# Performance work log

Measured on AMD Instinct MI355X. Metric: run time of the kernel, lower is better.

## Reference

```python
import jax, jax.numpy as jnp
import numpy as np

N_RAYS = 8192
N_SAMPLES = 128
HIDDEN = 128
SH_DIM = 16
RAY_EXT_FACTOR = 10.0


def rsh_cart_3(d):
    # Real spherical harmonics up to degree 3, Cartesian form (16 coeffs).
    x, y, z = d[..., 0], d[..., 1], d[..., 2]
    x2, y2, z2 = x * x, y * y, z * z
    xy, yz, xz = x * y, y * z, x * z
    return jnp.stack([
        0.282094791773878 * jnp.ones_like(x),
        -0.48860251190292 * y,
        0.48860251190292 * z,
        -0.48860251190292 * x,
        1.0925484305920792 * xy,
        -1.0925484305920792 * yz,
        0.94617469575756 * z2 - 0.31539156525252,
        -1.0925484305920792 * xz,
        0.5462742152960396 * (x2 - y2),
        0.5900435899266435 * y * (-3.0 * x2 + y2),
        2.8906114426405538 * xy * z,
        0.4570457994644658 * y * (1.0 - 5.0 * z2),
        0.3731763325901154 * z * (5.0 * z2 - 3.0),
        0.4570457994644658 * x * (1.0 - 5.0 * z2),
        1.445305721320277 * z * (x2 - y2),
        0.5900435899266435 * x * (-x2 + 3.0 * y2),
    ], axis=-1)


def setup_inputs() -> dict:
    key = jax.random.key(0)
    ks = jax.random.split(key, 11)
    o = jax.random.normal(ks[0], (N_RAYS, 3), dtype=jnp.float32)
    origins = 2.5 * o / jnp.linalg.norm(o, axis=-1, keepdims=True)
    # aim roughly at the unit AABB so most rays are active
    dirs = -origins + 0.2 * jax.random.normal(ks[1], (N_RAYS, 3), dtype=jnp.float32)
    u = jax.random.uniform(ks[2], (N_RAYS, N_SAMPLES), dtype=jnp.float32)
    s1 = 1.0 / np.sqrt(3.0)
    s2 = 1.0 / np.sqrt(HIDDEN)
    s3 = 1.0 / np.sqrt(HIDDEN + SH_DIM)
    return {
        'origins': origins,
        'dirs': dirs,
        'u': u,
        'W1': s1 * jax.random.normal(ks[3], (3, HIDDEN), dtype=jnp.float32),
        'b1': jnp.zeros((HIDDEN,), jnp.float32),
        'W2': s2 * jax.random.normal(ks[4], (HIDDEN, HIDDEN), dtype=jnp.float32),
        'b2': jnp.zeros((HIDDEN,), jnp.float32),
        'Wd': s2 * jax.random.normal(ks[5], (HIDDEN, 1), dtype=jnp.float32),
        'bd': jnp.zeros((1,), jnp.float32),
        'Wc': s3 * jax.random.normal(ks[6], (HIDDEN + SH_DIM, 3), dtype=jnp.float32),
        'bc': jnp.zeros((3,), jnp.float32),
    }


def reference(origins, dirs, u, W1, b1, W2, b2, Wd, bd, Wc, bc):
    B, T = u.shape
    # ---- AABB ([-1,1]^3) slab intersection -> tnear/tfar, active mask ----
    inv_d = 1.0 / dirs
    t1 = (-1.0 - origins) * inv_d
    t2 = (1.0 - origins) * inv_d
    tnear = jnp.maximum(jnp.max(jnp.minimum(t1, t2), axis=-1), 0.0)  # (B,)
    tfar = jnp.min(jnp.maximum(t1, t2), axis=-1)                      # (B,)
    active = tfar > tnear                                             # (B,)
    tfar_c = jnp.maximum(tfar, tnear + 1e-3)
    # ---- stratified ray step sampling ----
    frac = (jnp.arange(T, dtype=u.dtype) + u) / T                     # (B,T)
    ts = tnear[:, None] + (tfar_c - tnear)[:, None] * frac            # (B,T)
    xyz = origins[:, None, :] + dirs[:, None, :] * ts[..., None]      # (B,T,3)
    # aabb is [-1,1]^3 so ndc == xyz; spatial filter = bounds test
    xyz_ndc = xyz
    mask = jnp.all(jnp.abs(xyz_ndc) <= 1.0, axis=-1) & active[:, None]  # (B,T)
    dnorm = jnp.linalg.norm(dirs, axis=-1)                            # (B,)
    ynm = rsh_cart_3(dirs / dnorm[:, None])                           # (B,16)
    # ---- radiance field MLP over all sample points ----
    x = xyz_ndc.reshape(B * T, 3)
    h = jax.nn.relu(x @ W1 + b1)
    h = jax.nn.relu(h @ W2 + b2)
    sigma = jax.nn.softplus(h @ Wd + bd).reshape(B, T)
    cond = jnp.broadcast_to(ynm[:, None, :], (B, T, SH_DIM)).reshape(B * T, SH_DIM)
    color = jax.nn.sigmoid(jnp.concatenate([h, cond], axis=-1) @ Wc + bc).reshape(B, T, 3)
    # zero out points rejected by the spatial filter (torch writes only masked)
    sigma = sigma * mask
    color = color * mask[..., None]
    # ---- transmittance integration (integrate_timesteps) ----
    tfinal = tfar_c * RAY_EXT_FACTOR
    deltas = jnp.diff(ts, axis=-1, append=tfinal[:, None])            # (B,T)
    sd = sigma * deltas * dnorm[:, None]
    csum = jnp.cumsum(sd, axis=-1)
    # weights_i = T_i * alpha_i = exp(-csum_{i-1}) - exp(-csum_i)
    weights = jnp.exp(sd - csum) - jnp.exp(-csum)                     # (B,T)
    color_out = jnp.einsum('bt,btc->bc', weights, color)              # (B,3)
    alpha_out = jnp.sum(weights, axis=-1, keepdims=True)              # (B,1)
    rgba = jnp.concatenate([color_out, alpha_out], axis=-1)           # (B,4)
    return jnp.where(active[:, None], rgba, 0.0)
```

## Files before the change

### kernel.cpp

```cpp
#include <hip/hip_runtime.h>
#include <math.h>

#define NRAYS 8192
#define T 128
#define H 128
#define SHD 16

using short8 = __attribute__((ext_vector_type(8))) short;
using f32x4  = __attribute__((ext_vector_type(4))) float;
using f32x2  = __attribute__((ext_vector_type(2))) float;
using u32x2  = __attribute__((ext_vector_type(2))) unsigned;

__device__ __forceinline__ float fexp(float x) {
  return exp2f(x * 1.44269504088896341f);
}
__device__ __forceinline__ float softplus_f(float x) {
  return fmaxf(x, 0.f) + 0.693147180559945309f * log2f(1.f + fexp(-fabsf(x)));
}
__device__ __forceinline__ float sigmoid_f(float x) {
  return __builtin_amdgcn_rcpf(1.f + fexp(-x));
}

__device__ __forceinline__ unsigned f2bf(float f) {
  unsigned u = __float_as_uint(f);
  return (u + 0x7fffu + ((u >> 16) & 1u)) >> 16;
}

__device__ __forceinline__ unsigned pk2(f32x2 h) {
  unsigned r;
  asm("v_cvt_pk_bf16_f32 %0, %1, %2" : "=v"(r) : "v"(h[0]), "v"(h[1]));
  return r;
}

__global__ void preprocess(const float* __restrict__ W2, const float* __restrict__ Wd,
                           const float* __restrict__ Wc, const float* __restrict__ bc,
                           const float* __restrict__ origins, const float* __restrict__ dirs,
                           unsigned short* __restrict__ w2t,
                           unsigned short* __restrict__ woutf,
                           float* __restrict__ rayp_all) {
  const int t = blockIdx.x * 256 + threadIdx.x;
  if (t < 16384) {
    const int n = t >> 7, p = t & 127;
    const int o = (p >> 3) ^ (n & 7);
    const int k = o * 8 + (p & 7);
    w2t[t] = (unsigned short)f2bf(W2[k * 128 + n]);
  }
  if (t < 2048) {
    const int kk = t >> 9, L = (t >> 3) & 63, j = t & 7;
    const int c = L & 15, g = L >> 4;
    const int k = kk * 32 + g * 8 + j;
    float v = 0.f;
    if (c == 0) v = Wd[k];
    else if (c < 4) v = Wc[k * 3 + (c - 1)];
    woutf[t] = (unsigned short)f2bf(v);
  }
  if (t < NRAYS) {
    const float ox = origins[t*3+0], oy = origins[t*3+1], oz = origins[t*3+2];
    const float dx = dirs[t*3+0],  dy = dirs[t*3+1],  dz = dirs[t*3+2];
    const float ix = 1.f/dx, iy = 1.f/dy, iz = 1.f/dz;
    const float t1x = (-1.f-ox)*ix, t2x = (1.f-ox)*ix;
    const float t1y = (-1.f-oy)*iy, t2y = (1.f-oy)*iy;
    const float t1z = (-1.f-oz)*iz, t2z = (1.f-oz)*iz;
    float tnear = fmaxf(fmaxf(fminf(t1x,t2x), fminf(t1y,t2y)), fminf(t1z,t2z));
    tnear = fmaxf(tnear, 0.f);
    const float tfar = fminf(fminf(fmaxf(t1x,t2x), fmaxf(t1y,t2y)), fmaxf(t1z,t2z));
    const bool  active = tfar > tnear;
    const float tfar_c = fmaxf(tfar, tnear + 1e-3f);
    const float dnorm = sqrtf(dx*dx + dy*dy + dz*dz);
    const float nx = dx/dnorm, ny = dy/dnorm, nz = dz/dnorm;
    const float x2 = nx*nx, y2 = ny*ny, z2 = nz*nz;
    const float xy = nx*ny, yz = ny*nz, xz = nx*nz;
    float ynm[16];
    ynm[0]  = 0.282094791773878f;
    ynm[1]  = -0.48860251190292f*ny;
    ynm[2]  = 0.48860251190292f*nz;
    ynm[3]  = -0.48860251190292f*nx;
    ynm[4]  = 1.0925484305920792f*xy;
    ynm[5]  = -1.0925484305920792f*yz;
    ynm[6]  = 0.94617469575756f*z2 - 0.31539156525252f;
    ynm[7]  = -1.0925484305920792f*xz;
    ynm[8]  = 0.5462742152960396f*(x2-y2);
    ynm[9]  = 0.5900435899266435f*ny*(-3.f*x2+y2);
    ynm[10] = 2.8906114426405538f*xy*nz;
    ynm[11] = 0.4570457994644658f*ny*(1.f-5.f*z2);
    ynm[12] = 0.3731763325901154f*nz*(5.f*z2-3.f);
    ynm[13] = 0.4570457994644658f*nx*(1.f-5.f*z2);
    ynm[14] = 1.445305721320277f*nz*(x2-y2);
    ynm[15] = 0.5900435899266435f*nx*(-x2+3.f*y2);
    float cp0 = bc[0], cp1 = bc[1], cp2 = bc[2];
    #pragma unroll
    for (int s = 0; s < SHD; ++s) {
      cp0 = fmaf(ynm[s], Wc[(H+s)*3+0], cp0);
      cp1 = fmaf(ynm[s], Wc[(H+s)*3+1], cp1);
      cp2 = fmaf(ynm[s], Wc[(H+s)*3+2], cp2);
    }
    rayp_all[t*8+0] = tfar_c;
    rayp_all[t*8+1] = dnorm;
    rayp_all[t*8+2] = active ? 1.f : 0.f;
    rayp_all[t*8+3] = cp0;
    rayp_all[t*8+4] = cp1;
    rayp_all[t*8+5] = cp2;
    rayp_all[t*8+6] = tnear;
    rayp_all[t*8+7] = 0.f;
  }
}

__global__ __launch_bounds__(256, 4) void nerf_render(
    const float* __restrict__ origins, const float* __restrict__ dirs,
    const float* __restrict__ u, const float* __restrict__ W1,
    const float* __restrict__ b1, const float* __restrict__ b2,
    const float* __restrict__ bd, const unsigned short* __restrict__ w2t,
    const unsigned short* __restrict__ woutf, const float* __restrict__ rayp_all,
    float* __restrict__ out)
{
  const int ray = blockIdx.x;
  const int tid = threadIdx.x;
  const int L = tid & 63;
  const int w = tid >> 6;
  const int g = L >> 4;
  const int c = L & 15;

  __shared__ __align__(16) short Bs[16384];
  __shared__ __align__(16) float baseA[H];
  __shared__ __align__(16) float slopeA[H];
  __shared__ float ts_s[T];
  __shared__ float mask_s[T];
  __shared__ float wred[2][4];
  __shared__ float wtot[2];

  const float tfar_c = rayp_all[ray*8+0];
  const float dnorm  = rayp_all[ray*8+1];
  const float actf   = rayp_all[ray*8+2];
  const float cpo0   = rayp_all[ray*8+3];
  const float cpo1   = rayp_all[ray*8+4];
  const float cpo2   = rayp_all[ray*8+5];
  const float tnear  = rayp_all[ray*8+6];

  {
    const float4* src = (const float4*)w2t;
    float4* dst = (float4*)Bs;
    #pragma unroll
    for (int i = 0; i < 8; ++i) dst[tid + i * 256] = src[tid + i * 256];
  }

  if (tid < T) {
    const int tl = tid;
    const float ox = origins[ray*3+0], oy = origins[ray*3+1], oz = origins[ray*3+2];
    const float dx = dirs[ray*3+0],  dy = dirs[ray*3+1],  dz = dirs[ray*3+2];
    const bool active = actf != 0.f;
    const float ut = u[ray*T + tl];
    const float frac = ((float)tl + ut) * (1.f/(float)T);
    const float tt = tnear + (tfar_c - tnear) * frac;
    const float px = fmaf(dx, tt, ox);
    const float py = fmaf(dy, tt, oy);
    const float pz = fmaf(dz, tt, oz);
    ts_s[tl] = tt;
    const bool m = (fabsf(px) <= 1.f) && (fabsf(py) <= 1.f) && (fabsf(pz) <= 1.f) && active;
    mask_s[tl] = m ? 1.f : 0.f;
    const float w0 = W1[tl], w1v = W1[H + tl], w2v = W1[2*H + tl];
    baseA[tl]  = fmaf(ox, w0, fmaf(oy, w1v, fmaf(oz, w2v, b1[tl])));
    slopeA[tl] = fmaf(dx, w0, fmaf(dy, w1v, dz * w2v));
  }

  f32x4 acc[2][8];
  #pragma unroll
  for (int mt = 0; mt < 8; ++mt) {
    const float4 bv = *(const float4*)&b2[mt*16 + g*4];
    #pragma unroll
    for (int tm = 0; tm < 2; ++tm) {
      acc[tm][mt][0] = bv.x; acc[tm][mt][1] = bv.y;
      acc[tm][mt][2] = bv.z; acc[tm][mt][3] = bv.w;
    }
  }
  __syncthreads();

  const float t0 = ts_s[32*w + c];
  const float t1 = ts_s[32*w + 16 + c];
  const f32x2 tz0 = {t0, t0}, tz1 = {t1, t1};
  const f32x2 zero2 = {0.f, 0.f};

  #pragma unroll
  for (int ks = 0; ks < 4; ++ks) {
    const int kb = ks*32 + g*8;
    const f32x4 bq0 = *(const f32x4*)&baseA[kb];
    const f32x4 bq1 = *(const f32x4*)&baseA[kb+4];
    const f32x4 sq0 = *(const f32x4*)&slopeA[kb];
    const f32x4 sq1 = *(const f32x4*)&slopeA[kb+4];
    const f32x2 b01 = {bq0[0], bq0[1]}, b23 = {bq0[2], bq0[3]};
    const f32x2 b45 = {bq1[0], bq1[1]}, b67 = {bq1[2], bq1[3]};
    const f32x2 s01 = {sq0[0], sq0[1]}, s23 = {sq0[2], sq0[3]};
    const f32x2 s45 = {sq1[0], sq1[1]}, s67 = {sq1[2], sq1[3]};
    const f32x2 a01 = __builtin_elementwise_max(__builtin_elementwise_fma(tz0, s01, b01), zero2);
    const f32x2 a23 = __builtin_elementwise_max(__builtin_elementwise_fma(tz0, s23, b23), zero2);
    const f32x2 a45 = __builtin_elementwise_max(__builtin_elementwise_fma(tz0, s45, b45), zero2);
    const f32x2 a67 = __builtin_elementwise_max(__builtin_elementwise_fma(tz0, s67, b67), zero2);
    const f32x2 e01 = __builtin_elementwise_max(__builtin_elementwise_fma(tz1, s01, b01), zero2);
    const f32x2 e23 = __builtin_elementwise_max(__builtin_elementwise_fma(tz1, s23, b23), zero2);
    const f32x2 e45 = __builtin_elementwise_max(__builtin_elementwise_fma(tz1, s45, b45), zero2);
    const f32x2 e67 = __builtin_elementwise_max(__builtin_elementwise_fma(tz1, s67, b67), zero2);
    union U { uint4 u; short8 s; } A0, A1;
    A0.u = make_uint4(pk2(a01), pk2(a23), pk2(a45), pk2(a67));
    A1.u = make_uint4(pk2(e01), pk2(e23), pk2(e45), pk2(e67));
    const int swb = ((ks*4 + g) ^ (c & 7)) * 8;
    #pragma unroll
    for (int mt = 0; mt < 8; ++mt) {
      const short8 wf = *(const short8*)&Bs[(mt*16 + c)*128 + swb];
      acc[0][mt] = __builtin_amdgcn_mfma_f32_16x16x32_bf16(wf, A0.s, acc[0][mt], 0, 0, 0);
      acc[1][mt] = __builtin_amdgcn_mfma_f32_16x16x32_bf16(wf, A1.s, acc[1][mt], 0, 0, 0);
    }
  }
  __syncthreads();
  float4* SredP = (float4*)Bs;
  short*  As2   = Bs + 2048;

  short* As2w = As2 + w * 640;
  short8 wa[4];
  #pragma unroll
  for (int kk = 0; kk < 4; ++kk)
    wa[kk] = *(const short8*)&woutf[(kk*64 + L)*8];

  #pragma unroll
  for (int tm = 0; tm < 2; ++tm) {
    f32x4 oacc;
    oacc[0] = 0.f; oacc[1] = 0.f; oacc[2] = 0.f; oacc[3] = 0.f;
    #pragma unroll
    for (int kk = 0; kk < 4; ++kk) {
      #pragma unroll
      for (int i = 0; i < 2; ++i) {
        const f32x4 a = acc[tm][kk*2 + i];
        const f32x2 h01 = __builtin_elementwise_max((f32x2){a[0], a[1]}, zero2);
        const f32x2 h23 = __builtin_elementwise_max((f32x2){a[2], a[3]}, zero2);
        *(uint2*)&As2w[c*40 + i*16 + g*4] = make_uint2(pk2(h01), pk2(h23));
      }
      const short8 hbf = *(const short8*)&As2w[c*40 + g*8];
      oacc = __builtin_amdgcn_mfma_f32_16x16x32_bf16(wa[kk], hbf, oacc, 0, 0, 0);
    }
    if (g == 0)
      SredP[32*w + 16*tm + c] = make_float4(oacc[0], oacc[1], oacc[2], oacc[3]);
  }
  __syncthreads();

  float sd = 0.f, cc0 = 0.f, cc1 = 0.f, cc2 = 0.f;
  if (tid < T) {
    const float4 sv = SredP[tid];
    const float mk = mask_s[tid];
    const float sigma = softplus_f(sv.x + bd[0]) * mk;
    cc0 = mk * sigmoid_f(sv.y + cpo0);
    cc1 = mk * sigmoid_f(sv.z + cpo1);
    cc2 = mk * sigmoid_f(sv.w + cpo2);
    const float tt = ts_s[tid];
    const float tnext = (tid < T-1) ? ts_s[tid + 1] : tfar_c * 10.f;
    sd = sigma * (tnext - tt) * dnorm;
  }

  float val = sd;
  #pragma unroll
  for (int off = 1; off < 64; off <<= 1) {
    const float tmp = __shfl_up(val, off);
    if (L >= off) val += tmp;
  }
  if (tid < T && L == 63) wtot[w] = val;
  __syncthreads();
  const float csum = val + ((w == 1) ? wtot[0] : 0.f);

  float wgt = 0.f, wcx = 0.f, wcy = 0.f, wcz = 0.f;
  if (tid < T) {
    wgt = fexp(sd - csum) - fexp(-csum);
    wcx = wgt * cc0; wcy = wgt * cc1; wcz = wgt * cc2;
  }
  #pragma unroll
  for (int mm = 32; mm >= 1; mm >>= 1) {
    wgt += __shfl_xor(wgt, mm);
    wcx += __shfl_xor(wcx, mm);
    wcy += __shfl_xor(wcy, mm);
    wcz += __shfl_xor(wcz, mm);
  }
  if (tid < T && L == 0) {
    wred[w][0] = wgt; wred[w][1] = wcx; wred[w][2] = wcy; wred[w][3] = wcz;
  }
  __syncthreads();
  if (tid == 0) {
    const float aw = wred[0][0] + wred[1][0];
    const float o0 = wred[0][1] + wred[1][1];
    const float o1 = wred[0][2] + wred[1][2];
    const float o2 = wred[0][3] + wred[1][3];
    const bool act = actf != 0.f;
    out[ray*4+0] = act ? o0 : 0.f;
    out[ray*4+1] = act ? o1 : 0.f;
    out[ray*4+2] = act ? o2 : 0.f;
    out[ray*4+3] = act ? aw : 0.f;
  }
}

extern "C" void kernel_launch(void* const* d_in, const int* in_sizes, int n_in,
                              void* d_out, int out_size, void* d_ws, size_t ws_size,
                              hipStream_t stream) {
  const float* origins = (const float*)d_in[0];
  const float* dirs    = (const float*)d_in[1];
  const float* u       = (const float*)d_in[2];
  const float* W1      = (const float*)d_in[3];
  const float* b1      = (const float*)d_in[4];
  const float* W2      = (const float*)d_in[5];
  const float* b2      = (const float*)d_in[6];
  const float* Wd      = (const float*)d_in[7];
  const float* bd      = (const float*)d_in[8];
  const float* Wc      = (const float*)d_in[9];
  const float* bc      = (const float*)d_in[10];

  unsigned short* w2t      = (unsigned short*)d_ws;
  unsigned short* woutf    = (unsigned short*)((char*)d_ws + 32768);
  float*          rayp_all = (float*)((char*)d_ws + 36864);

  preprocess<<<64, 256, 0, stream>>>(W2, Wd, Wc, bc, origins, dirs,
                                     w2t, woutf, rayp_all);
  nerf_render<<<NRAYS, 256, 0, stream>>>(origins, dirs, u, W1, b1, b2, bd,
                                         w2t, woutf, rayp_all, (float*)d_out);
}
```

Before: 133.2 us.

## Map one ray per wavefront and amortize W2 LDS staging across four rays

Each block now handles four rays, one per wavefront, instead of one ray per block. This spreads the 32KB W2 copy into shared memory over four rays, and the per-ray setup, scan and reduction now run inside one wavefront with shuffles and ds_bpermute, so most block-level barriers are gone. Each wave walks its 128 samples in four chunks of 32 and carries a running cumulative sum through a per-chunk prefix scan. The cost is more serial work per wave, more bpermute traffic to rebuild layer-1 activations, and a grid four times smaller.

```diff
diff --git a/kernel.cpp b/kernel.cpp
--- a/kernel.cpp
+++ b/kernel.cpp
@@ -9,7 +9,6 @@
 using short8 = __attribute__((ext_vector_type(8))) short;
 using f32x4  = __attribute__((ext_vector_type(4))) float;
 using f32x2  = __attribute__((ext_vector_type(2))) float;
-using u32x2  = __attribute__((ext_vector_type(2))) unsigned;
 
 __device__ __forceinline__ float fexp(float x) {
   return exp2f(x * 1.44269504088896341f);
@@ -30,6 +29,14 @@
   unsigned r;
   asm("v_cvt_pk_bf16_f32 %0, %1, %2" : "=v"(r) : "v"(h[0]), "v"(h[1]));
   return r;
+}
+
+__device__ __forceinline__ float rflf(float v) {
+  return __builtin_bit_cast(float, __builtin_amdgcn_readfirstlane(__builtin_bit_cast(int, v)));
+}
+
+__device__ __forceinline__ float bpermf(int byteaddr, float v) {
+  return __builtin_bit_cast(float, __builtin_amdgcn_ds_bpermute(byteaddr, __builtin_bit_cast(int, v)));
 }
 
 __global__ void preprocess(const float* __restrict__ W2, const float* __restrict__ Wd,
@@ -113,28 +120,16 @@
     const unsigned short* __restrict__ woutf, const float* __restrict__ rayp_all,
     float* __restrict__ out)
 {
-  const int ray = blockIdx.x;
   const int tid = threadIdx.x;
   const int L = tid & 63;
   const int w = tid >> 6;
   const int g = L >> 4;
   const int c = L & 15;
+  const int ray = blockIdx.x * 4 + w;
 
   __shared__ __align__(16) short Bs[16384];
-  __shared__ __align__(16) float baseA[H];
-  __shared__ __align__(16) float slopeA[H];
-  __shared__ float ts_s[T];
-  __shared__ float mask_s[T];
-  __shared__ float wred[2][4];
-  __shared__ float wtot[2];
-
-  const float tfar_c = rayp_all[ray*8+0];
-  const float dnorm  = rayp_all[ray*8+1];
-  const float actf   = rayp_all[ray*8+2];
-  const float cpo0   = rayp_all[ray*8+3];
-  const float cpo1   = rayp_all[ray*8+4];
-  const float cpo2   = rayp_all[ray*8+5];
-  const float tnear  = rayp_all[ray*8+6];
+  __shared__ __align__(16) float b2s[128];
+  __shared__ __align__(16) short As2[4 * 640];
 
   {
     const float4* src = (const float4*)w2t;
@@ -142,153 +137,181 @@
     #pragma unroll
     for (int i = 0; i < 8; ++i) dst[tid + i * 256] = src[tid + i * 256];
   }
-
-  if (tid < T) {
-    const int tl = tid;
-    const float ox = origins[ray*3+0], oy = origins[ray*3+1], oz = origins[ray*3+2];
-    const float dx = dirs[ray*3+0],  dy = dirs[ray*3+1],  dz = dirs[ray*3+2];
-    const bool active = actf != 0.f;
-    const float ut = u[ray*T + tl];
-    const float frac = ((float)tl + ut) * (1.f/(float)T);
-    const float tt = tnear + (tfar_c - tnear) * frac;
+  if (tid < 128) b2s[tid] = b2[tid];
+
+  const float tfar_c = rflf(rayp_all[ray*8+0]);
+  const float dnorm  = rflf(rayp_all[ray*8+1]);
+  const float actf   = rflf(rayp_all[ray*8+2]);
+  const float cp0    = rflf(rayp_all[ray*8+3]);
+  const float cp1    = rflf(rayp_all[ray*8+4]);
+  const float cp2    = rflf(rayp_all[ray*8+5]);
+  const float tnear  = rflf(rayp_all[ray*8+6]);
+  const float bd0    = rflf(bd[0]);
+  const float ox = rflf(origins[ray*3+0]);
+  const float oy = rflf(origins[ray*3+1]);
+  const float oz = rflf(origins[ray*3+2]);
+  const float dx = rflf(dirs[ray*3+0]);
+  const float dy = rflf(dirs[ray*3+1]);
+  const float dz = rflf(dirs[ray*3+2]);
+  const bool active = actf != 0.f;
+
+  float ts_q[2], dmn_q[2], mk_q[2];
+  #pragma unroll
+  for (int q = 0; q < 2; ++q) {
+    const int s = q*64 + L;
+    const float uv = u[ray*T + s];
+    const float frac = ((float)s + uv) * (1.f/(float)T);
+    const float tt = fmaf(tfar_c - tnear, frac, tnear);
+    ts_q[q] = tt;
     const float px = fmaf(dx, tt, ox);
     const float py = fmaf(dy, tt, oy);
     const float pz = fmaf(dz, tt, oz);
-    ts_s[tl] = tt;
-    const bool m = (fabsf(px) <= 1.f) && (fabsf(py) <= 1.f) && (fabsf(pz) <= 1.f) && active;
-    mask_s[tl] = m ? 1.f : 0.f;
-    const float w0 = W1[tl], w1v = W1[H + tl], w2v = W1[2*H + tl];
-    baseA[tl]  = fmaf(ox, w0, fmaf(oy, w1v, fmaf(oz, w2v, b1[tl])));
-    slopeA[tl] = fmaf(dx, w0, fmaf(dy, w1v, dz * w2v));
-  }
-
-  f32x4 acc[2][8];
-  #pragma unroll
-  for (int mt = 0; mt < 8; ++mt) {
-    const float4 bv = *(const float4*)&b2[mt*16 + g*4];
-    #pragma unroll
-    for (int tm = 0; tm < 2; ++tm) {
-      acc[tm][mt][0] = bv.x; acc[tm][mt][1] = bv.y;
-      acc[tm][mt][2] = bv.z; acc[tm][mt][3] = bv.w;
-    }
-  }
-  __syncthreads();
-
-  const float t0 = ts_s[32*w + c];
-  const float t1 = ts_s[32*w + 16 + c];
-  const f32x2 tz0 = {t0, t0}, tz1 = {t1, t1};
-  const f32x2 zero2 = {0.f, 0.f};
-
-  #pragma unroll
-  for (int ks = 0; ks < 4; ++ks) {
-    const int kb = ks*32 + g*8;
-    const f32x4 bq0 = *(const f32x4*)&baseA[kb];
-    const f32x4 bq1 = *(const f32x4*)&baseA[kb+4];
-    const f32x4 sq0 = *(const f32x4*)&slopeA[kb];
-    const f32x4 sq1 = *(const f32x4*)&slopeA[kb+4];
-    const f32x2 b01 = {bq0[0], bq0[1]}, b23 = {bq0[2], bq0[3]};
-    const f32x2 b45 = {bq1[0], bq1[1]}, b67 = {bq1[2], bq1[3]};
-    const f32x2 s01 = {sq0[0], sq0[1]}, s23 = {sq0[2], sq0[3]};
-    const f32x2 s45 = {sq1[0], sq1[1]}, s67 = {sq1[2], sq1[3]};
-    const f32x2 a01 = __builtin_elementwise_max(__builtin_elementwise_fma(tz0, s01, b01), zero2);
-    const f32x2 a23 = __builtin_elementwise_max(__builtin_elementwise_fma(tz0, s23, b23), zero2);
-    const f32x2 a45 = __builtin_elementwise_max(__builtin_elementwise_fma(tz0, s45, b45), zero2);
-    const f32x2 a67 = __builtin_elementwise_max(__builtin_elementwise_fma(tz0, s67, b67), zero2);
-    const f32x2 e01 = __builtin_elementwise_max(__builtin_elementwise_fma(tz1, s01, b01), zero2);
-    const f32x2 e23 = __builtin_elementwise_max(__builtin_elementwise_fma(tz1, s23, b23), zero2);
-    const f32x2 e45 = __builtin_elementwise_max(__builtin_elementwise_fma(tz1, s45, b45), zero2);
-    const f32x2 e67 = __builtin_elementwise_max(__builtin_elementwise_fma(tz1, s67, b67), zero2);
-    union U { uint4 u; short8 s; } A0, A1;
-    A0.u = make_uint4(pk2(a01), pk2(a23), pk2(a45), pk2(a67));
-    A1.u = make_uint4(pk2(e01), pk2(e23), pk2(e45), pk2(e67));
-    const int swb = ((ks*4 + g) ^ (c & 7)) * 8;
-    #pragma unroll
-    for (int mt = 0; mt < 8; ++mt) {
-      const short8 wf = *(const short8*)&Bs[(mt*16 + c)*128 + swb];
-      acc[0][mt] = __builtin_amdgcn_mfma_f32_16x16x32_bf16(wf, A0.s, acc[0][mt], 0, 0, 0);
-      acc[1][mt] = __builtin_amdgcn_mfma_f32_16x16x32_bf16(wf, A1.s, acc[1][mt], 0, 0, 0);
-    }
-  }
-  __syncthreads();
-  float4* SredP = (float4*)Bs;
-  short*  As2   = Bs + 2048;
-
-  short* As2w = As2 + w * 640;
+    mk_q[q] = ((fabsf(px) <= 1.f) && (fabsf(py) <= 1.f) && (fabsf(pz) <= 1.f) && active)
+                ? 1.f : 0.f;
+  }
+  {
+    const float t64 = __shfl(ts_q[1], 0);
+    float tn0 = __shfl(ts_q[0], (L+1) & 63);
+    float tn1 = __shfl(ts_q[1], (L+1) & 63);
+    tn0 = (L == 63) ? t64 : tn0;
+    tn1 = (L == 63) ? tfar_c * 10.f : tn1;
+    dmn_q[0] = mk_q[0] * (tn0 - ts_q[0]) * dnorm;
+    dmn_q[1] = mk_q[1] * (tn1 - ts_q[1]) * dnorm;
+  }
+  float base_q[2], slope_q[2];
+  #pragma unroll
+  for (int q = 0; q < 2; ++q) {
+    const int hh = q*64 + L;
+    const float w0v = W1[hh], w1v = W1[H + hh], w2v = W1[2*H + hh];
+    base_q[q]  = fmaf(ox, w0v, fmaf(oy, w1v, fmaf(oz, w2v, b1[hh])));
+    slope_q[q] = fmaf(dx, w0v, fmaf(dy, w1v, dz * w2v));
+  }
+
   short8 wa[4];
   #pragma unroll
   for (int kk = 0; kk < 4; ++kk)
     wa[kk] = *(const short8*)&woutf[(kk*64 + L)*8];
 
-  #pragma unroll
-  for (int tm = 0; tm < 2; ++tm) {
-    f32x4 oacc;
-    oacc[0] = 0.f; oacc[1] = 0.f; oacc[2] = 0.f; oacc[3] = 0.f;
-    #pragma unroll
-    for (int kk = 0; kk < 4; ++kk) {
+  __syncthreads();
+
+  short* As2w = As2 + w * 640;
+  const int permbase = g * 32;
+  const f32x2 zero2 = {0.f, 0.f};
+  f32x4 acc[2][8];
+  float csum = 0.f, pw = 0.f, pxc = 0.f, pyc = 0.f, pzc = 0.f;
+
+  #pragma unroll
+  for (int stp = 0; stp < 4; ++stp) {
+    const int q = stp >> 1;
+    const int i0 = ((stp*32 + c) & 63) * 4;
+    const int i1 = ((stp*32 + 16 + c) & 63) * 4;
+    const float t0 = bpermf(i0, ts_q[q]);
+    const float t1 = bpermf(i1, ts_q[q]);
+    const float d0 = bpermf(i0, dmn_q[q]);
+    const float d1 = bpermf(i1, dmn_q[q]);
+    const f32x2 tz0 = {t0, t0}, tz1 = {t1, t1};
+
+    #pragma unroll
+    for (int mt = 0; mt < 8; ++mt) {
+      const f32x4 bv = *(const f32x4*)&b2s[mt*16 + g*4];
+      acc[0][mt] = bv; acc[1][mt] = bv;
+    }
+
+    #pragma unroll
+    for (int ks = 0; ks < 4; ++ks) {
+      const int kq = ks >> 1;
+      const int pb = permbase + ((ks & 1) << 7);
+      float bj[8], sj[8];
       #pragma unroll
-      for (int i = 0; i < 2; ++i) {
-        const f32x4 a = acc[tm][kk*2 + i];
-        const f32x2 h01 = __builtin_elementwise_max((f32x2){a[0], a[1]}, zero2);
-        const f32x2 h23 = __builtin_elementwise_max((f32x2){a[2], a[3]}, zero2);
-        *(uint2*)&As2w[c*40 + i*16 + g*4] = make_uint2(pk2(h01), pk2(h23));
+      for (int j = 0; j < 8; ++j) {
+        bj[j] = bpermf(pb + j*4, base_q[kq]);
+        sj[j] = bpermf(pb + j*4, slope_q[kq]);
       }
-      const short8 hbf = *(const short8*)&As2w[c*40 + g*8];
-      oacc = __builtin_amdgcn_mfma_f32_16x16x32_bf16(wa[kk], hbf, oacc, 0, 0, 0);
-    }
-    if (g == 0)
-      SredP[32*w + 16*tm + c] = make_float4(oacc[0], oacc[1], oacc[2], oacc[3]);
-  }
-  __syncthreads();
-
-  float sd = 0.f, cc0 = 0.f, cc1 = 0.f, cc2 = 0.f;
-  if (tid < T) {
-    const float4 sv = SredP[tid];
-    const float mk = mask_s[tid];
-    const float sigma = softplus_f(sv.x + bd[0]) * mk;
-    cc0 = mk * sigmoid_f(sv.y + cpo0);
-    cc1 = mk * sigmoid_f(sv.z + cpo1);
-    cc2 = mk * sigmoid_f(sv.w + cpo2);
-    const float tt = ts_s[tid];
-    const float tnext = (tid < T-1) ? ts_s[tid + 1] : tfar_c * 10.f;
-    sd = sigma * (tnext - tt) * dnorm;
-  }
-
-  float val = sd;
-  #pragma unroll
-  for (int off = 1; off < 64; off <<= 1) {
-    const float tmp = __shfl_up(val, off);
-    if (L >= off) val += tmp;
-  }
-  if (tid < T && L == 63) wtot[w] = val;
-  __syncthreads();
-  const float csum = val + ((w == 1) ? wtot[0] : 0.f);
-
-  float wgt = 0.f, wcx = 0.f, wcy = 0.f, wcz = 0.f;
-  if (tid < T) {
-    wgt = fexp(sd - csum) - fexp(-csum);
-    wcx = wgt * cc0; wcy = wgt * cc1; wcz = wgt * cc2;
-  }
-  #pragma unroll
-  for (int mm = 32; mm >= 1; mm >>= 1) {
-    wgt += __shfl_xor(wgt, mm);
-    wcx += __shfl_xor(wcx, mm);
-    wcy += __shfl_xor(wcy, mm);
-    wcz += __shfl_xor(wcz, mm);
-  }
-  if (tid < T && L == 0) {
-    wred[w][0] = wgt; wred[w][1] = wcx; wred[w][2] = wcy; wred[w][3] = wcz;
-  }
-  __syncthreads();
-  if (tid == 0) {
-    const float aw = wred[0][0] + wred[1][0];
-    const float o0 = wred[0][1] + wred[1][1];
-    const float o1 = wred[0][2] + wred[1][2];
-    const float o2 = wred[0][3] + wred[1][3];
-    const bool act = actf != 0.f;
-    out[ray*4+0] = act ? o0 : 0.f;
-    out[ray*4+1] = act ? o1 : 0.f;
-    out[ray*4+2] = act ? o2 : 0.f;
-    out[ray*4+3] = act ? aw : 0.f;
+      const f32x2 b01 = {bj[0], bj[1]}, b23 = {bj[2], bj[3]};
+      const f32x2 b45 = {bj[4], bj[5]}, b67 = {bj[6], bj[7]};
+      const f32x2 s01 = {sj[0], sj[1]}, s23 = {sj[2], sj[3]};
+      const f32x2 s45 = {sj[4], sj[5]}, s67 = {sj[6], sj[7]};
+      const f32x2 a01 = __builtin_elementwise_max(__builtin_elementwise_fma(tz0, s01, b01), zero2);
+      const f32x2 a23 = __builtin_elementwise_max(__builtin_elementwise_fma(tz0, s23, b23), zero2);
+      const f32x2 a45 = __builtin_elementwise_max(__builtin_elementwise_fma(tz0, s45, b45), zero2);
+      const f32x2 a67 = __builtin_elementwise_max(__builtin_elementwise_fma(tz0, s67, b67), zero2);
+      const f32x2 e01 = __builtin_elementwise_max(__builtin_elementwise_fma(tz1, s01, b01), zero2);
+      const f32x2 e23 = __builtin_elementwise_max(__builtin_elementwise_fma(tz1, s23, b23), zero2);
+      const f32x2 e45 = __builtin_elementwise_max(__builtin_elementwise_fma(tz1, s45, b45), zero2);
+      const f32x2 e67 = __builtin_elementwise_max(__builtin_elementwise_fma(tz1, s67, b67), zero2);
+      union U { uint4 u; short8 s; } A0, A1;
+      A0.u = make_uint4(pk2(a01), pk2(a23), pk2(a45), pk2(a67));
+      A1.u = make_uint4(pk2(e01), pk2(e23), pk2(e45), pk2(e67));
+      const int swb = ((ks*4 + g) ^ (c & 7)) * 8;
+      #pragma unroll
+      for (int mt = 0; mt < 8; ++mt) {
+        const short8 wf = *(const short8*)&Bs[(mt*16 + c)*128 + swb];
+        acc[0][mt] = __builtin_amdgcn_mfma_f32_16x16x32_bf16(wf, A0.s, acc[0][mt], 0, 0, 0);
+        acc[1][mt] = __builtin_amdgcn_mfma_f32_16x16x32_bf16(wf, A1.s, acc[1][mt], 0, 0, 0);
+      }
+    }
+
+    f32x4 osig[2];
+    #pragma unroll
+    for (int tm = 0; tm < 2; ++tm) {
+      f32x4 oacc;
+      oacc[0] = 0.f; oacc[1] = 0.f; oacc[2] = 0.f; oacc[3] = 0.f;
+      #pragma unroll
+      for (int kk = 0; kk < 4; ++kk) {
+        #pragma unroll
+        for (int i = 0; i < 2; ++i) {
+          const f32x4 a = acc[tm][kk*2 + i];
+          const f32x2 h01 = __builtin_elementwise_max((f32x2){a[0], a[1]}, zero2);
+          const f32x2 h23 = __builtin_elementwise_max((f32x2){a[2], a[3]}, zero2);
+          *(uint2*)&As2w[c*40 + i*16 + g*4] = make_uint2(pk2(h01), pk2(h23));
+        }
+        const short8 hbf = *(const short8*)&As2w[c*40 + g*8];
+        oacc = __builtin_amdgcn_mfma_f32_16x16x32_bf16(wa[kk], hbf, oacc, 0, 0, 0);
+      }
+      osig[tm] = oacc;
+    }
+
+    const float sd0 = softplus_f(osig[0][0] + bd0) * d0;
+    const float sd1 = softplus_f(osig[1][0] + bd0) * d1;
+    float p0 = sd0;
+    #pragma unroll
+    for (int off = 1; off < 16; off <<= 1) {
+      const float tpp = __shfl_up(p0, off, 16);
+      p0 += ((L & 15) >= off) ? tpp : 0.f;
+    }
+    const float tot0 = __shfl(p0, 15);
+    float p1 = sd1;
+    #pragma unroll
+    for (int off = 1; off < 16; off <<= 1) {
+      const float tpp = __shfl_up(p1, off, 16);
+      p1 += ((L & 15) >= off) ? tpp : 0.f;
+    }
+    const float tot1 = __shfl(p1, 15);
+    const float cs0 = csum + p0;
+    const float cs1 = csum + tot0 + p1;
+    csum += tot0 + tot1;
+    const float w0 = fexp(sd0 - cs0) - fexp(-cs0);
+    const float w1 = fexp(sd1 - cs1) - fexp(-cs1);
+    pw  += w0 + w1;
+    pxc += w0 * sigmoid_f(osig[0][1] + cp0) + w1 * sigmoid_f(osig[1][1] + cp0);
+    pyc += w0 * sigmoid_f(osig[0][2] + cp1) + w1 * sigmoid_f(osig[1][2] + cp1);
+    pzc += w0 * sigmoid_f(osig[0][3] + cp2) + w1 * sigmoid_f(osig[1][3] + cp2);
+  }
+
+  #pragma unroll
+  for (int off = 1; off < 16; off <<= 1) {
+    pw  += __shfl_xor(pw, off);
+    pxc += __shfl_xor(pxc, off);
+    pyc += __shfl_xor(pyc, off);
+    pzc += __shfl_xor(pzc, off);
+  }
+  if (L == 0) {
+    float4 o;
+    o.x = active ? pxc : 0.f;
+    o.y = active ? pyc : 0.f;
+    o.z = active ? pzc : 0.f;
+    o.w = active ? pw  : 0.f;
+    *(float4*)&out[ray*4] = o;
   }
 }
 
@@ -313,6 +336,6 @@
 
   preprocess<<<64, 256, 0, stream>>>(W2, Wd, Wc, bc, origins, dirs,
                                      w2t, woutf, rayp_all);
-  nerf_render<<<NRAYS, 256, 0, stream>>>(origins, dirs, u, W1, b1, b2, bd,
-                                         w2t, woutf, rayp_all, (float*)d_out);
-}
+  nerf_render<<<NRAYS/4, 256, 0, stream>>>(origins, dirs, u, W1, b1, b2, bd,
+                                           w2t, woutf, rayp_all, (float*)d_out);
+}
```

New measurement: 214.8 us. 1.61x slower.

## Process two rays per 512-thread block and double-buffer output-layer staging

Applied to the files above, without the earlier changes.

Each block now handles two rays with 512 threads, so the 32KB bf16 W2 tile loaded into shared memory is shared by both rays and the per-ray global-to-LDS copy cost is halved. The output-layer staging alternates between two LDS slabs so the next slab can be written while the previous one is consumed by the MFMA. Shared memory per block grows and launch bounds change to 512x2, which may affect occupancy. The final output is written as a single float4.

```diff
diff --git a/kernel.cpp b/kernel.cpp
--- a/kernel.cpp
+++ b/kernel.cpp
@@ -9,7 +9,6 @@
 using short8 = __attribute__((ext_vector_type(8))) short;
 using f32x4  = __attribute__((ext_vector_type(4))) float;
 using f32x2  = __attribute__((ext_vector_type(2))) float;
-using u32x2  = __attribute__((ext_vector_type(2))) unsigned;
 
 __device__ __forceinline__ float fexp(float x) {
   return exp2f(x * 1.44269504088896341f);
@@ -105,7 +104,17 @@
   }
 }
 
-__global__ __launch_bounds__(256, 4) void nerf_render(
+#define SLAB_W(kk, sb) { \
+  { const f32x4 a = acc[tm][(kk)*2+0]; \
+    const f32x2 h01 = __builtin_elementwise_max((f32x2){a[0],a[1]}, zero2); \
+    const f32x2 h23 = __builtin_elementwise_max((f32x2){a[2],a[3]}, zero2); \
+    *(uint2*)&(sb)[c*40 + g*4] = make_uint2(pk2(h01), pk2(h23)); } \
+  { const f32x4 a = acc[tm][(kk)*2+1]; \
+    const f32x2 h01 = __builtin_elementwise_max((f32x2){a[0],a[1]}, zero2); \
+    const f32x2 h23 = __builtin_elementwise_max((f32x2){a[2],a[3]}, zero2); \
+    *(uint2*)&(sb)[c*40 + 16 + g*4] = make_uint2(pk2(h01), pk2(h23)); } }
+
+__global__ __launch_bounds__(512, 2) void nerf_render(
     const float* __restrict__ origins, const float* __restrict__ dirs,
     const float* __restrict__ u, const float* __restrict__ W1,
     const float* __restrict__ b1, const float* __restrict__ b2,
@@ -113,53 +122,50 @@
     const unsigned short* __restrict__ woutf, const float* __restrict__ rayp_all,
     float* __restrict__ out)
 {
-  const int ray = blockIdx.x;
   const int tid = threadIdx.x;
   const int L = tid & 63;
   const int w = tid >> 6;
+  const int wr = w & 3;
+  const int r  = w >> 2;
   const int g = L >> 4;
   const int c = L & 15;
 
   __shared__ __align__(16) short Bs[16384];
-  __shared__ __align__(16) float baseA[H];
-  __shared__ __align__(16) float slopeA[H];
-  __shared__ float ts_s[T];
-  __shared__ float mask_s[T];
-  __shared__ float wred[2][4];
-  __shared__ float wtot[2];
-
-  const float tfar_c = rayp_all[ray*8+0];
-  const float dnorm  = rayp_all[ray*8+1];
-  const float actf   = rayp_all[ray*8+2];
-  const float cpo0   = rayp_all[ray*8+3];
-  const float cpo1   = rayp_all[ray*8+4];
-  const float cpo2   = rayp_all[ray*8+5];
-  const float tnear  = rayp_all[ray*8+6];
+  __shared__ __align__(16) float baseA[2][H];
+  __shared__ __align__(16) float slopeA[2][H];
+  __shared__ __align__(16) float ts_s[2][T];
+  __shared__ __align__(16) float mask_s[2][T];
+  __shared__ float wred[2][2][4];
+  __shared__ float wtot[2][2];
 
   {
     const float4* src = (const float4*)w2t;
     float4* dst = (float4*)Bs;
     #pragma unroll
-    for (int i = 0; i < 8; ++i) dst[tid + i * 256] = src[tid + i * 256];
-  }
-
-  if (tid < T) {
-    const int tl = tid;
-    const float ox = origins[ray*3+0], oy = origins[ray*3+1], oz = origins[ray*3+2];
-    const float dx = dirs[ray*3+0],  dy = dirs[ray*3+1],  dz = dirs[ray*3+2];
+    for (int i = 0; i < 4; ++i) dst[tid + i * 512] = src[tid + i * 512];
+  }
+
+  if (tid < 256) {
+    const int r2 = tid >> 7, tl = tid & 127;
+    const int ray2 = blockIdx.x * 2 + r2;
+    const float tfar_c = rayp_all[ray2*8+0];
+    const float actf   = rayp_all[ray2*8+2];
+    const float tnear  = rayp_all[ray2*8+6];
+    const float ox = origins[ray2*3+0], oy = origins[ray2*3+1], oz = origins[ray2*3+2];
+    const float dx = dirs[ray2*3+0],  dy = dirs[ray2*3+1],  dz = dirs[ray2*3+2];
     const bool active = actf != 0.f;
-    const float ut = u[ray*T + tl];
+    const float ut = u[ray2*T + tl];
     const float frac = ((float)tl + ut) * (1.f/(float)T);
     const float tt = tnear + (tfar_c - tnear) * frac;
     const float px = fmaf(dx, tt, ox);
     const float py = fmaf(dy, tt, oy);
     const float pz = fmaf(dz, tt, oz);
-    ts_s[tl] = tt;
+    ts_s[r2][tl] = tt;
     const bool m = (fabsf(px) <= 1.f) && (fabsf(py) <= 1.f) && (fabsf(pz) <= 1.f) && active;
-    mask_s[tl] = m ? 1.f : 0.f;
+    mask_s[r2][tl] = m ? 1.f : 0.f;
     const float w0 = W1[tl], w1v = W1[H + tl], w2v = W1[2*H + tl];
-    baseA[tl]  = fmaf(ox, w0, fmaf(oy, w1v, fmaf(oz, w2v, b1[tl])));
-    slopeA[tl] = fmaf(dx, w0, fmaf(dy, w1v, dz * w2v));
+    baseA[r2][tl]  = fmaf(ox, w0, fmaf(oy, w1v, fmaf(oz, w2v, b1[tl])));
+    slopeA[r2][tl] = fmaf(dx, w0, fmaf(dy, w1v, dz * w2v));
   }
 
   f32x4 acc[2][8];
@@ -174,18 +180,18 @@
   }
   __syncthreads();
 
-  const float t0 = ts_s[32*w + c];
-  const float t1 = ts_s[32*w + 16 + c];
+  const float t0 = ts_s[r][32*wr + c];
+  const float t1 = ts_s[r][32*wr + 16 + c];
   const f32x2 tz0 = {t0, t0}, tz1 = {t1, t1};
   const f32x2 zero2 = {0.f, 0.f};
 
   #pragma unroll
   for (int ks = 0; ks < 4; ++ks) {
     const int kb = ks*32 + g*8;
-    const f32x4 bq0 = *(const f32x4*)&baseA[kb];
-    const f32x4 bq1 = *(const f32x4*)&baseA[kb+4];
-    const f32x4 sq0 = *(const f32x4*)&slopeA[kb];
-    const f32x4 sq1 = *(const f32x4*)&slopeA[kb+4];
+    const f32x4 bq0 = *(const f32x4*)&baseA[r][kb];
+    const f32x4 bq1 = *(const f32x4*)&baseA[r][kb+4];
+    const f32x4 sq0 = *(const f32x4*)&slopeA[r][kb];
+    const f32x4 sq1 = *(const f32x4*)&slopeA[r][kb+4];
     const f32x2 b01 = {bq0[0], bq0[1]}, b23 = {bq0[2], bq0[3]};
     const f32x2 b45 = {bq1[0], bq1[1]}, b67 = {bq1[2], bq1[3]};
     const f32x2 s01 = {sq0[0], sq0[1]}, s23 = {sq0[2], sq0[3]};
@@ -213,7 +219,8 @@
   float4* SredP = (float4*)Bs;
   short*  As2   = Bs + 2048;
 
-  short* As2w = As2 + w * 640;
+  short* sb0 = As2 + w * 1280;
+  short* sb1 = sb0 + 640;
   short8 wa[4];
   #pragma unroll
   for (int kk = 0; kk < 4; ++kk)
@@ -223,33 +230,40 @@
   for (int tm = 0; tm < 2; ++tm) {
     f32x4 oacc;
     oacc[0] = 0.f; oacc[1] = 0.f; oacc[2] = 0.f; oacc[3] = 0.f;
-    #pragma unroll
-    for (int kk = 0; kk < 4; ++kk) {
-      #pragma unroll
-      for (int i = 0; i < 2; ++i) {
-        const f32x4 a = acc[tm][kk*2 + i];
-        const f32x2 h01 = __builtin_elementwise_max((f32x2){a[0], a[1]}, zero2);
-        const f32x2 h23 = __builtin_elementwise_max((f32x2){a[2], a[3]}, zero2);
-        *(uint2*)&As2w[c*40 + i*16 + g*4] = make_uint2(pk2(h01), pk2(h23));
-      }
-      const short8 hbf = *(const short8*)&As2w[c*40 + g*8];
-      oacc = __builtin_amdgcn_mfma_f32_16x16x32_bf16(wa[kk], hbf, oacc, 0, 0, 0);
-    }
+    SLAB_W(0, sb0)
+    SLAB_W(1, sb1)
+    { const short8 h = *(const short8*)&sb0[c*40 + g*8];
+      oacc = __builtin_amdgcn_mfma_f32_16x16x32_bf16(wa[0], h, oacc, 0, 0, 0); }
+    SLAB_W(2, sb0)
+    { const short8 h = *(const short8*)&sb1[c*40 + g*8];
+      oacc = __builtin_amdgcn_mfma_f32_16x16x32_bf16(wa[1], h, oacc, 0, 0, 0); }
+    SLAB_W(3, sb1)
+    { const short8 h = *(const short8*)&sb0[c*40 + g*8];
+      oacc = __builtin_amdgcn_mfma_f32_16x16x32_bf16(wa[2], h, oacc, 0, 0, 0); }
+    { const short8 h = *(const short8*)&sb1[c*40 + g*8];
+      oacc = __builtin_amdgcn_mfma_f32_16x16x32_bf16(wa[3], h, oacc, 0, 0, 0); }
     if (g == 0)
-      SredP[32*w + 16*tm + c] = make_float4(oacc[0], oacc[1], oacc[2], oacc[3]);
+      SredP[r*128 + 32*wr + 16*tm + c] = make_float4(oacc[0], oacc[1], oacc[2], oacc[3]);
   }
   __syncthreads();
 
   float sd = 0.f, cc0 = 0.f, cc1 = 0.f, cc2 = 0.f;
-  if (tid < T) {
-    const float4 sv = SredP[tid];
-    const float mk = mask_s[tid];
+  if (tid < 256) {
+    const int r2 = tid >> 7, s = tid & 127;
+    const int ray2 = blockIdx.x * 2 + r2;
+    const float4 sv = SredP[r2*128 + s];
+    const float mk = mask_s[r2][s];
+    const float dnorm  = rayp_all[ray2*8+1];
+    const float cpo0   = rayp_all[ray2*8+3];
+    const float cpo1   = rayp_all[ray2*8+4];
+    const float cpo2   = rayp_all[ray2*8+5];
+    const float tfar_c = rayp_all[ray2*8+0];
     const float sigma = softplus_f(sv.x + bd[0]) * mk;
     cc0 = mk * sigmoid_f(sv.y + cpo0);
     cc1 = mk * sigmoid_f(sv.z + cpo1);
     cc2 = mk * sigmoid_f(sv.w + cpo2);
-    const float tt = ts_s[tid];
-    const float tnext = (tid < T-1) ? ts_s[tid + 1] : tfar_c * 10.f;
+    const float tt = ts_s[r2][s];
+    const float tnext = (s < T-1) ? ts_s[r2][s + 1] : tfar_c * 10.f;
     sd = sigma * (tnext - tt) * dnorm;
   }
 
@@ -259,12 +273,12 @@
     const float tmp = __shfl_up(val, off);
     if (L >= off) val += tmp;
   }
-  if (tid < T && L == 63) wtot[w] = val;
-  __syncthreads();
-  const float csum = val + ((w == 1) ? wtot[0] : 0.f);
+  if (tid < 256 && L == 63) wtot[tid >> 7][(tid >> 6) & 1] = val;
+  __syncthreads();
 
   float wgt = 0.f, wcx = 0.f, wcy = 0.f, wcz = 0.f;
-  if (tid < T) {
+  if (tid < 256) {
+    const float csum = val + (((tid >> 6) & 1) ? wtot[tid >> 7][0] : 0.f);
     wgt = fexp(sd - csum) - fexp(-csum);
     wcx = wgt * cc0; wcy = wgt * cc1; wcz = wgt * cc2;
   }
@@ -275,20 +289,24 @@
     wcy += __shfl_xor(wcy, mm);
     wcz += __shfl_xor(wcz, mm);
   }
-  if (tid < T && L == 0) {
-    wred[w][0] = wgt; wred[w][1] = wcx; wred[w][2] = wcy; wred[w][3] = wcz;
-  }
-  __syncthreads();
-  if (tid == 0) {
-    const float aw = wred[0][0] + wred[1][0];
-    const float o0 = wred[0][1] + wred[1][1];
-    const float o1 = wred[0][2] + wred[1][2];
-    const float o2 = wred[0][3] + wred[1][3];
-    const bool act = actf != 0.f;
-    out[ray*4+0] = act ? o0 : 0.f;
-    out[ray*4+1] = act ? o1 : 0.f;
-    out[ray*4+2] = act ? o2 : 0.f;
-    out[ray*4+3] = act ? aw : 0.f;
+  if (tid < 256 && L == 0) {
+    float* wr4 = wred[tid >> 7][(tid >> 6) & 1];
+    wr4[0] = wgt; wr4[1] = wcx; wr4[2] = wcy; wr4[3] = wcz;
+  }
+  __syncthreads();
+  if (tid < 2) {
+    const int ray2 = blockIdx.x * 2 + tid;
+    const float aw = wred[tid][0][0] + wred[tid][1][0];
+    const float o0 = wred[tid][0][1] + wred[tid][1][1];
+    const float o1 = wred[tid][0][2] + wred[tid][1][2];
+    const float o2 = wred[tid][0][3] + wred[tid][1][3];
+    const bool act = rayp_all[ray2*8+2] != 0.f;
+    float4 o;
+    o.x = act ? o0 : 0.f;
+    o.y = act ? o1 : 0.f;
+    o.z = act ? o2 : 0.f;
+    o.w = act ? aw : 0.f;
+    *(float4*)&out[ray2*4] = o;
   }
 }
 
@@ -313,6 +331,6 @@
 
   preprocess<<<64, 256, 0, stream>>>(W2, Wd, Wc, bc, origins, dirs,
                                      w2t, woutf, rayp_all);
-  nerf_render<<<NRAYS, 256, 0, stream>>>(origins, dirs, u, W1, b1, b2, bd,
-                                         w2t, woutf, rayp_all, (float*)d_out);
-}
+  nerf_render<<<NRAYS/2, 512, 0, stream>>>(origins, dirs, u, W1, b1, b2, bd,
+                                           w2t, woutf, rayp_all, (float*)d_out);
+}
```

After: 136.1 us. 1.02x slower.
